# Performance work log

Hardware: AMD Instinct MI355X
Metric: run time of the kernel (lower is better)

The kernel has to match this reference:

```python
import jax, jax.numpy as jnp
import numpy as np

N = 50000      # nodes
E_RAND = 600000  # random edges per meta-path
M = 3          # meta-paths
D_IN = 128
D_OUT = 128
H_SEM = 128    # SemanticAttention hidden (default 128)
NEG_SLOPE = 0.2  # DGL GATConv leaky_relu default


def setup_inputs() -> dict:
    key = jax.random.key(0)
    ks = jax.random.split(key, 12)
    h = jax.random.normal(ks[0], (N, D_IN), dtype=jnp.float32)
    src = jax.random.randint(ks[1], (M, E_RAND), 0, N, dtype=jnp.int32)
    dst = jax.random.randint(ks[2], (M, E_RAND), 0, N, dtype=jnp.int32)
    # add self-loops (dgl.add_self_loop): guarantees every dst has >=1 edge
    loops = jnp.broadcast_to(jnp.arange(N, dtype=jnp.int32), (M, N))
    edge_src = jnp.concatenate([src, loops], axis=1)
    edge_dst = jnp.concatenate([dst, loops], axis=1)
    W_gat = jax.random.normal(ks[3], (M, D_IN, D_OUT), dtype=jnp.float32) * 0.05
    attn_l = jax.random.normal(ks[4], (M, D_OUT), dtype=jnp.float32) * 0.1
    attn_r = jax.random.normal(ks[5], (M, D_OUT), dtype=jnp.float32) * 0.1
    bias_gat = jax.random.normal(ks[6], (M, D_OUT), dtype=jnp.float32) * 0.02
    Ws1 = jax.random.normal(ks[7], (D_OUT, H_SEM), dtype=jnp.float32) * 0.05
    bs1 = jnp.zeros((H_SEM,), dtype=jnp.float32)
    Ws2 = jax.random.normal(ks[8], (H_SEM,), dtype=jnp.float32) * 0.05
    return {"h": h, "edge_src": edge_src, "edge_dst": edge_dst,
            "W_gat": W_gat, "attn_l": attn_l, "attn_r": attn_r,
            "bias_gat": bias_gat, "Ws1": Ws1, "bs1": bs1, "Ws2": Ws2}


def _gat_meta_path(feat_m, el_m, er_m, src, dst):
    # feat_m: [N, D]; el/er: [N]; src/dst: [E]
    e = jax.nn.leaky_relu(el_m[src] + er_m[dst], NEG_SLOPE)  # [E]
    emax = jax.ops.segment_max(e, dst, num_segments=N)       # [N]
    ex = jnp.exp(e - emax[dst])
    denom = jax.ops.segment_sum(ex, dst, num_segments=N)     # [N]
    a = ex / denom[dst]                                      # edge softmax
    # scatter-aggregate weighted source features -> [N, D]
    return jax.ops.segment_sum(a[:, None] * feat_m[src], dst, num_segments=N)


def reference(h, edge_src, edge_dst, W_gat, attn_l, attn_r, bias_gat, Ws1, bs1, Ws2):
    # per-meta-path GATConv projections
    feat = jnp.einsum('ni,mio->mno', h, W_gat)            # [M, N, D]
    el = jnp.einsum('mno,mo->mn', feat, attn_l)           # [M, N]
    er = jnp.einsum('mno,mo->mn', feat, attn_r)           # [M, N]
    z = jax.vmap(_gat_meta_path)(feat, el, er, edge_src, edge_dst)  # [M, N, D]
    z = jax.nn.elu(z + bias_gat[:, None, :])              # GATConv bias + activation
    z = jnp.transpose(z, (1, 0, 2))                       # [N, M, D]
    # SemanticAttention: Linear -> tanh -> Linear(no bias), mean over nodes, softmax over meta-paths
    w = jnp.einsum('nmh,h->nm', jnp.tanh(jnp.einsum('nmd,dh->nmh', z, Ws1) + bs1), Ws2)
    beta = jax.nn.softmax(w.mean(0))                      # [M]
    return jnp.einsum('m,nmd->nd', beta, z)               # [N, D]
```

## Files before the change

### kernel.cpp

```cpp
#include <hip/hip_runtime.h>
#include <hip/hip_fp16.h>

#define NV 50000
#define EE 650000
#define MM 3
#define NBUK 49
#define CHSZ 4096
#define NCH 159
#define SEMBLK 586

typedef __attribute__((ext_vector_type(8))) __bf16 bf16x8;
typedef __attribute__((ext_vector_type(8))) _Float16 f16x8;
typedef __attribute__((ext_vector_type(8))) unsigned short u16x8;
typedef __attribute__((ext_vector_type(4))) float f32x4;

__device__ __forceinline__ unsigned short f2bf(float f) {
    unsigned u = __builtin_bit_cast(unsigned, f);
    u += 0x7FFFu + ((u >> 16) & 1u);
    return (unsigned short)(u >> 16);
}
__device__ __forceinline__ float bflo(unsigned v) {
    unsigned x = v << 16; return __builtin_bit_cast(float, x);
}
__device__ __forceinline__ float bfhi(unsigned v) {
    unsigned x = v & 0xFFFF0000u; return __builtin_bit_cast(float, x);
}
__device__ __forceinline__ bf16x8 zero8() {
    u16x8 u = {0,0,0,0,0,0,0,0};
    return __builtin_bit_cast(bf16x8, u);
}
__device__ __forceinline__ f16x8 zero8h() {
    u16x8 u = {0,0,0,0,0,0,0,0};
    return __builtin_bit_cast(f16x8, u);
}
__device__ __forceinline__ unsigned short f2h(float f) {
    return __builtin_bit_cast(unsigned short, __float2half(f));
}
__device__ __forceinline__ float h2f(unsigned short u) {
    return __half2float(__builtin_bit_cast(__half, u));
}

__global__ void prep_wt(const float* __restrict__ Wg, const float* __restrict__ Ws1,
                        unsigned short* __restrict__ WT, unsigned short* __restrict__ WsT) {
    int idx = blockIdx.x * 256 + threadIdx.x;
    if (idx < MM * 16384) {
        int m = idx / 16384, r = idx % 16384;
        int o = r >> 7, d = r & 127;
        WT[idx] = f2bf(Wg[m * 16384 + d * 128 + o]);
    } else {
        int r = idx - MM * 16384;
        int j = r >> 7, d = r & 127;
        WsT[r] = f2h(Ws1[d * 128 + j]);
    }
}

__global__ void prep_h(const float* __restrict__ h, unsigned* __restrict__ hb) {
    int idx = blockIdx.x * 256 + threadIdx.x;
    if (idx < NV * 64) {
        float2 f = *reinterpret_cast<const float2*>(h + (size_t)idx * 2);
        hb[idx] = ((unsigned)f2bf(f.x)) | (((unsigned)f2bf(f.y)) << 16);
    }
}

__global__ __launch_bounds__(256, 2) void gemm_feat(
    const unsigned short* __restrict__ hb, const unsigned short* __restrict__ WT,
    const float* __restrict__ attn_l, const float* __restrict__ attn_r,
    unsigned* __restrict__ featb, float* __restrict__ el, float* __restrict__ er) {
    const int m = blockIdx.y;
    const int tid = threadIdx.x;
    const int wave = tid >> 6, lane = tid & 63;
    const int lo = lane & 15, hi = lane >> 4;
    const int rowbase = blockIdx.x * 256 + wave * 64;
    const unsigned short* WTm = WT + m * 16384;

    f32x4 acc[4][8];
#pragma unroll
    for (int a = 0; a < 4; ++a)
#pragma unroll
        for (int b = 0; b < 8; ++b) acc[a][b] = (f32x4){0.f, 0.f, 0.f, 0.f};

#pragma unroll
    for (int kk = 0; kk < 4; ++kk) {
        bf16x8 bfrag[8];
#pragma unroll
        for (int ct = 0; ct < 8; ++ct)
            bfrag[ct] = *reinterpret_cast<const bf16x8*>(WTm + (ct * 16 + lo) * 128 + kk * 32 + hi * 8);
#pragma unroll
        for (int rt = 0; rt < 4; ++rt) {
            int row = rowbase + rt * 16 + lo;
            bf16x8 af = (row < NV)
                ? *reinterpret_cast<const bf16x8*>(hb + (size_t)row * 128 + kk * 32 + hi * 8)
                : zero8();
#pragma unroll
            for (int ct = 0; ct < 8; ++ct)
                acc[rt][ct] = __builtin_amdgcn_mfma_f32_16x16x32_bf16(af, bfrag[ct], acc[rt][ct], 0, 0, 0);
        }
    }

    float alv[8], arv[8];
#pragma unroll
    for (int ct = 0; ct < 8; ++ct) {
        alv[ct] = attn_l[m * 128 + ct * 16 + lo];
        arv[ct] = attn_r[m * 128 + ct * 16 + lo];
    }

#pragma unroll
    for (int rt = 0; rt < 4; ++rt) {
        float pl[4] = {0.f, 0.f, 0.f, 0.f}, pr[4] = {0.f, 0.f, 0.f, 0.f};
#pragma unroll
        for (int ct = 0; ct < 8; ++ct)
#pragma unroll
            for (int i = 0; i < 4; ++i) {
                pl[i] += acc[rt][ct][i] * alv[ct];
                pr[i] += acc[rt][ct][i] * arv[ct];
            }
#pragma unroll
        for (int s = 1; s < 16; s <<= 1)
#pragma unroll
            for (int i = 0; i < 4; ++i) {
                pl[i] += __shfl_xor(pl[i], s, 64);
                pr[i] += __shfl_xor(pr[i], s, 64);
            }
        int row0 = rowbase + rt * 16 + hi * 4;
        if (lo == 0) {
#pragma unroll
            for (int i = 0; i < 4; ++i)
                if (row0 + i < NV) {
                    el[m * NV + row0 + i] = pl[i];
                    er[m * NV + row0 + i] = pr[i];
                }
        }
#pragma unroll
        for (int ct = 0; ct < 8; ++ct)
#pragma unroll
            for (int i = 0; i < 4; ++i) {
                float v = acc[rt][ct][i];
                float vp = __shfl_xor(v, 1, 64);
                int row = row0 + i;
                if (((lo & 1) == 0) && row < NV) {
                    unsigned pk = ((unsigned)f2bf(v)) | (((unsigned)f2bf(vp)) << 16);
                    featb[(size_t)(m * NV + row) * 64 + ct * 8 + (lo >> 1)] = pk;
                }
            }
    }
}

__global__ __launch_bounds__(256) void hist_k(const int* __restrict__ edst,
                                              int* __restrict__ counts) {
    int m = blockIdx.y, c = blockIdx.x, tid = threadIdx.x;
    __shared__ int hsm[NBUK];
    if (tid < NBUK) hsm[tid] = 0;
    __syncthreads();
    int base = c * CHSZ;
#pragma unroll
    for (int i = 0; i < CHSZ / 256; ++i) {
        int e = base + i * 256 + tid;
        if (e < EE) {
            int d = edst[(size_t)m * EE + e];
            atomicAdd(&hsm[d >> 10], 1);
        }
    }
    __syncthreads();
    if (tid < NBUK) counts[(m * NCH + c) * NBUK + tid] = hsm[tid];
}

__global__ __launch_bounds__(256) void scan_k(const int* __restrict__ counts,
                                              int* __restrict__ chunkpos,
                                              int* __restrict__ bstart) {
    int t = threadIdx.x;
    __shared__ int btot[MM * NBUK];
    if (t < MM * NBUK) {
        int m = t / NBUK, b = t % NBUK;
        int run = 0;
        for (int c = 0; c < NCH; ++c) {
            chunkpos[(m * NCH + c) * NBUK + b] = run;
            run += counts[(m * NCH + c) * NBUK + b];
        }
        btot[t] = run;
    }
    __syncthreads();
    if (t == 0) {
        for (int m = 0; m < MM; ++m) {
            int run = 0;
            for (int b = 0; b < NBUK; ++b) {
                bstart[m * NBUK + b] = run;
                run += btot[m * NBUK + b];
            }
        }
    }
}

__global__ __launch_bounds__(256) void scat1_k(const int* __restrict__ esrc,
                                               const int* __restrict__ edst,
                                               const int* __restrict__ chunkpos,
                                               const int* __restrict__ bstart,
                                               unsigned* __restrict__ staging) {
    int m = blockIdx.y, c = blockIdx.x, tid = threadIdx.x;
    __shared__ int cnt[NBUK];
    __shared__ int sofs[NBUK];
    if (tid < NBUK) {
        cnt[tid] = 0;
        sofs[tid] = bstart[m * NBUK + tid] + chunkpos[(m * NCH + c) * NBUK + tid];
    }
    __syncthreads();
    int base = c * CHSZ;
#pragma unroll
    for (int i = 0; i < CHSZ / 256; ++i) {
        int e = base + i * 256 + tid;
        if (e < EE) {
            int s = esrc[(size_t)m * EE + e];
            int d = edst[(size_t)m * EE + e];
            int b = d >> 10;
            int r = atomicAdd(&cnt[b], 1);
            staging[(size_t)m * EE + sofs[b] + r] =
                ((unsigned)(d & 1023) << 16) | (unsigned)s;
        }
    }
}

__global__ __launch_bounds__(1024) void bsort_k(const unsigned* __restrict__ staging,
                                                const int* __restrict__ bstart,
                                                const float* __restrict__ el,
                                                const float* __restrict__ er,
                                                unsigned* __restrict__ csr,
                                                int* __restrict__ start,
                                                int* __restrict__ deg) {
    int b = blockIdx.x, m = blockIdx.y, t = threadIdx.x;
    __shared__ int hsm[1024];
    __shared__ int sc[1024];
    __shared__ int cur[1024];
    hsm[t] = 0;
    __syncthreads();
    int sbase = bstart[m * NBUK + b];
    int nseg = ((b == NBUK - 1) ? EE : bstart[m * NBUK + b + 1]) - sbase;
    const unsigned* sp = staging + (size_t)m * EE + sbase;
    for (int i = t; i < nseg; i += 1024)
        atomicAdd(&hsm[sp[i] >> 16], 1);
    __syncthreads();
    int v = hsm[t];
    sc[t] = v;
    __syncthreads();
#pragma unroll
    for (int s = 1; s < 1024; s <<= 1) {
        int add = (t >= s) ? sc[t - s] : 0;
        __syncthreads();
        sc[t] += add;
        __syncthreads();
    }
    int excl = sc[t] - v;
    cur[t] = excl;
    int node = (b << 10) + t;
    if (node < NV) {
        deg[m * NV + node] = v;
        start[m * NV + node] = sbase + excl;
    }
    __syncthreads();
    unsigned* cp = csr + (size_t)m * EE + sbase;
    int node0 = b << 10;
    for (int i = t; i < nseg; i += 1024) {
        unsigned rec = sp[i];
        int dloc = rec >> 16;
        int s = rec & 0xFFFF;
        float x = el[m * NV + s] + er[m * NV + node0 + dloc];
        x = x > 0.f ? x : 0.2f * x;
        float ex = __expf(x);
        int slot = atomicAdd(&cur[dloc], 1);
        cp[slot] = ((unsigned)f2h(ex) << 16) | (unsigned)s;
    }
}

__global__ __launch_bounds__(256) void aggregate_k(
    const unsigned* __restrict__ featb, const unsigned* __restrict__ csr,
    const int* __restrict__ start, const int* __restrict__ deg,
    const float* __restrict__ bias, unsigned* __restrict__ zh) {
    int wid = blockIdx.x * 4 + (threadIdx.x >> 6);
    int gw = wid * 2 + ((threadIdx.x >> 5) & 1);
    int sl = threadIdx.x & 31;
    int m = gw / NV;
    int st = start[gw];
    int dg = deg[gw];
    const unsigned* pp = csr + (size_t)m * EE + st;
    const unsigned* fb = featb + (size_t)m * NV * 64 + sl * 2;
    float2 a01 = {0.f, 0.f}, a23 = {0.f, 0.f};
    float den = 0.f;
    int full = dg & ~7;
    int e0 = 0;
    for (; e0 < full; e0 += 8) {
        unsigned p[8];
#pragma unroll
        for (int i = 0; i < 8; ++i) p[i] = pp[e0 + i];
        uint2 v[8];
#pragma unroll
        for (int i = 0; i < 8; ++i)
            v[i] = *reinterpret_cast<const uint2*>(fb + (size_t)(p[i] & 0xFFFF) * 64);
#pragma unroll
        for (int i = 0; i < 8; ++i) {
            float x = h2f((unsigned short)(p[i] >> 16));
            a01.x += x * bflo(v[i].x); a01.y += x * bfhi(v[i].x);
            a23.x += x * bflo(v[i].y); a23.y += x * bfhi(v[i].y);
            den += x;
        }
    }
    if (e0 < dg) {
        int dgm1 = dg - 1;
        unsigned p[8];
#pragma unroll
        for (int i = 0; i < 8; ++i) p[i] = pp[min(e0 + i, dgm1)];
        uint2 v[8];
#pragma unroll
        for (int i = 0; i < 8; ++i)
            v[i] = *reinterpret_cast<const uint2*>(fb + (size_t)(p[i] & 0xFFFF) * 64);
#pragma unroll
        for (int i = 0; i < 8; ++i) {
            float x = (e0 + i < dg) ? h2f((unsigned short)(p[i] >> 16)) : 0.f;
            a01.x += x * bflo(v[i].x); a01.y += x * bfhi(v[i].x);
            a23.x += x * bflo(v[i].y); a23.y += x * bfhi(v[i].y);
            den += x;
        }
    }
    float inv = 1.f / den;
    int d0 = sl * 4;
    const float* bp = bias + m * 128 + d0;
    float z0 = a01.x * inv + bp[0];
    float z1 = a01.y * inv + bp[1];
    float z2 = a23.x * inv + bp[2];
    float z3 = a23.y * inv + bp[3];
    z0 = z0 > 0.f ? z0 : (__expf(z0) - 1.f);
    z1 = z1 > 0.f ? z1 : (__expf(z1) - 1.f);
    z2 = z2 > 0.f ? z2 : (__expf(z2) - 1.f);
    z3 = z3 > 0.f ? z3 : (__expf(z3) - 1.f);
    uint2 o;
    o.x = ((unsigned)f2h(z0)) | (((unsigned)f2h(z1)) << 16);
    o.y = ((unsigned)f2h(z2)) | (((unsigned)f2h(z3)) << 16);
    *reinterpret_cast<uint2*>(zh + (size_t)gw * 64 + sl * 2) = o;
}

__global__ __launch_bounds__(256, 2) void semantic_k(
    const unsigned* __restrict__ zh, const unsigned short* __restrict__ WsT,
    const float* __restrict__ bs1, const float* __restrict__ Ws2,
    float* __restrict__ wpart) {
    const int tid = threadIdx.x;
    const int wave = tid >> 6, lane = tid & 63;
    const int lo = lane & 15, hi = lane >> 4;
    const int rowbase = blockIdx.x * 256 + wave * 64;

    f32x4 acc[4][8];
#pragma unroll
    for (int a = 0; a < 4; ++a)
#pragma unroll
        for (int b = 0; b < 8; ++b) acc[a][b] = (f32x4){0.f, 0.f, 0.f, 0.f};

#pragma unroll
    for (int kk = 0; kk < 4; ++kk) {
        f16x8 bfrag[8];
#pragma unroll
        for (int ct = 0; ct < 8; ++ct)
            bfrag[ct] = *reinterpret_cast<const f16x8*>(WsT + (ct * 16 + lo) * 128 + kk * 32 + hi * 8);
#pragma unroll
        for (int rt = 0; rt < 4; ++rt) {
            int row = rowbase + rt * 16 + lo;
            f16x8 af = (row < MM * NV)
                ? *reinterpret_cast<const f16x8*>(zh + (size_t)row * 64 + kk * 16 + hi * 2)
                : zero8h();
#pragma unroll
            for (int ct = 0; ct < 8; ++ct)
                acc[rt][ct] = __builtin_amdgcn_mfma_f32_16x16x32_f16(af, bfrag[ct], acc[rt][ct], 0, 0, 0);
        }
    }

    float w2v[8], b1v[8];
#pragma unroll
    for (int ct = 0; ct < 8; ++ct) {
        w2v[ct] = Ws2[ct * 16 + lo];
        b1v[ct] = bs1[ct * 16 + lo];
    }

    float t0 = 0.f, t1 = 0.f, t2 = 0.f;
#pragma unroll
    for (int rt = 0; rt < 4; ++rt) {
        int rbase = rowbase + rt * 16;
        if (rbase >= MM * NV) continue;
        int mm = rbase / NV;
        float p = 0.f;
#pragma unroll
        for (int ct = 0; ct < 8; ++ct)
#pragma unroll
            for (int i = 0; i < 4; ++i) {
                float x = acc[rt][ct][i] + b1v[ct];
                x = fminf(fmaxf(x, -15.f), 15.f);
                float t = __expf(2.f * x);
                p += w2v[ct] * ((t - 1.f) / (t + 1.f));
            }
#pragma unroll
        for (int s = 1; s < 64; s <<= 1) p += __shfl_xor(p, s, 64);
        if (mm == 0) t0 += p; else if (mm == 1) t1 += p; else t2 += p;
    }

    __shared__ float smw[4][3];
    if (lane == 0) { smw[wave][0] = t0; smw[wave][1] = t1; smw[wave][2] = t2; }
    __syncthreads();
    if (tid < 3)
        wpart[blockIdx.x * 4 + tid] =
            smw[0][tid] + smw[1][tid] + smw[2][tid] + smw[3][tid];
}

__global__ __launch_bounds__(64) void beta_k(const float* __restrict__ wpart,
                                             float* __restrict__ beta) {
    int lane = threadIdx.x;
    float t0 = 0.f, t1 = 0.f, t2 = 0.f;
    for (int b = lane; b < SEMBLK; b += 64) {
        t0 += wpart[b * 4 + 0];
        t1 += wpart[b * 4 + 1];
        t2 += wpart[b * 4 + 2];
    }
#pragma unroll
    for (int s = 1; s < 64; s <<= 1) {
        t0 += __shfl_xor(t0, s, 64);
        t1 += __shfl_xor(t1, s, 64);
        t2 += __shfl_xor(t2, s, 64);
    }
    if (lane == 0) {
        float w0 = t0 * (1.f / NV), w1 = t1 * (1.f / NV), w2 = t2 * (1.f / NV);
        float mx = fmaxf(w0, fmaxf(w1, w2));
        float e0 = __expf(w0 - mx), e1 = __expf(w1 - mx), e2 = __expf(w2 - mx);
        float inv = 1.f / (e0 + e1 + e2);
        beta[0] = e0 * inv; beta[1] = e1 * inv; beta[2] = e2 * inv;
    }
}

__global__ __launch_bounds__(256) void combine_k(const unsigned* __restrict__ zh,
                                                 const float* __restrict__ beta,
                                                 float* __restrict__ out) {
    int idx = blockIdx.x * 256 + threadIdx.x;
    float b0 = beta[0], b1 = beta[1], b2 = beta[2];
    uint2 u0 = *reinterpret_cast<const uint2*>(zh + (size_t)idx * 2);
    uint2 u1 = *reinterpret_cast<const uint2*>(zh + (size_t)NV * 64 + (size_t)idx * 2);
    uint2 u2 = *reinterpret_cast<const uint2*>(zh + (size_t)2 * NV * 64 + (size_t)idx * 2);
    float2 a0 = __half22float2(__builtin_bit_cast(__half2, u0.x));
    float2 a1 = __half22float2(__builtin_bit_cast(__half2, u0.y));
    float2 c0 = __half22float2(__builtin_bit_cast(__half2, u1.x));
    float2 c1 = __half22float2(__builtin_bit_cast(__half2, u1.y));
    float2 d0 = __half22float2(__builtin_bit_cast(__half2, u2.x));
    float2 d1 = __half22float2(__builtin_bit_cast(__half2, u2.y));
    float4 o;
    o.x = b0 * a0.x + b1 * c0.x + b2 * d0.x;
    o.y = b0 * a0.y + b1 * c0.y + b2 * d0.y;
    o.z = b0 * a1.x + b1 * c1.x + b2 * d1.x;
    o.w = b0 * a1.y + b1 * c1.y + b2 * d1.y;
    *reinterpret_cast<float4*>(out + (size_t)idx * 4) = o;
}

extern "C" void kernel_launch(void* const* d_in, const int* in_sizes, int n_in,
                              void* d_out, int out_size, void* d_ws, size_t ws_size,
                              hipStream_t stream) {
    const float* h      = (const float*)d_in[0];
    const int*   esrc   = (const int*)d_in[1];
    const int*   edst   = (const int*)d_in[2];
    const float* Wg     = (const float*)d_in[3];
    const float* attn_l = (const float*)d_in[4];
    const float* attn_r = (const float*)d_in[5];
    const float* bias   = (const float*)d_in[6];
    const float* Ws1    = (const float*)d_in[7];
    const float* bs1    = (const float*)d_in[8];
    const float* Ws2    = (const float*)d_in[9];
    float* out = (float*)d_out;

    char* w = (char*)d_ws;
    auto alloc = [&](size_t bytes) { char* p = w; w += (bytes + 255) & ~(size_t)255; return p; };
    unsigned short* WT   = (unsigned short*)alloc((size_t)MM * 128 * 128 * 2);
    unsigned short* WsT  = (unsigned short*)alloc((size_t)128 * 128 * 2);
    unsigned* hb    = (unsigned*)alloc((size_t)NV * 64 * 4);
    unsigned* featb = (unsigned*)alloc((size_t)MM * NV * 64 * 4);
    unsigned* zh    = (unsigned*)alloc((size_t)MM * NV * 64 * 4);
    float* el     = (float*)alloc((size_t)MM * NV * 4);
    float* er     = (float*)alloc((size_t)MM * NV * 4);
    int*   deg    = (int*)alloc((size_t)MM * NV * 4);
    int*   startb = (int*)alloc((size_t)MM * NV * 4);
    int*   counts = (int*)alloc((size_t)MM * NCH * NBUK * 4);
    int*   chunkpos = (int*)alloc((size_t)MM * NCH * NBUK * 4);
    int*   bstart = (int*)alloc((size_t)MM * NBUK * 4);
    unsigned* staging = (unsigned*)alloc((size_t)MM * EE * 4);
    unsigned* csr     = (unsigned*)alloc((size_t)MM * EE * 4);
    float* wpart  = (float*)alloc((size_t)SEMBLK * 4 * 4);
    float* beta   = (float*)alloc(256);

    hipLaunchKernelGGL(prep_wt, dim3(256), dim3(256), 0, stream, Wg, Ws1, WT, WsT);
    hipLaunchKernelGGL(prep_h, dim3((NV * 64 + 255) / 256), dim3(256), 0, stream, h, hb);
    hipLaunchKernelGGL(gemm_feat, dim3(196, MM), dim3(256), 0, stream,
                       (const unsigned short*)hb, WT, attn_l, attn_r, featb, el, er);
    hipLaunchKernelGGL(hist_k, dim3(NCH, MM), dim3(256), 0, stream, edst, counts);
    hipLaunchKernelGGL(scan_k, dim3(1), dim3(256), 0, stream, counts, chunkpos, bstart);
    hipLaunchKernelGGL(scat1_k, dim3(NCH, MM), dim3(256), 0, stream,
                       esrc, edst, chunkpos, bstart, staging);
    hipLaunchKernelGGL(bsort_k, dim3(NBUK, MM), dim3(1024), 0, stream,
                       staging, bstart, el, er, csr, startb, deg);
    hipLaunchKernelGGL(aggregate_k, dim3((MM * NV) / 8), dim3(256), 0, stream,
                       featb, csr, startb, deg, bias, zh);
    hipLaunchKernelGGL(semantic_k, dim3(SEMBLK), dim3(256), 0, stream,
                       zh, WsT, bs1, Ws2, wpart);
    hipLaunchKernelGGL(beta_k, dim3(1), dim3(64), 0, stream, wpart, beta);
    hipLaunchKernelGGL(combine_k, dim3(6250), dim3(256), 0, stream, zh, beta, out);
}
```

Before: 233.5 us.

## Pad CSR segments to multiples of 8, use fp16 features, finer buckets, merged prep

Each node's CSR segment is now padded to a multiple of 8 entries, with zero-weight filler records and aligned per-bucket offsets. This lets the aggregation loop use vectorized uint4 index loads and drop its masked tail iteration. Buckets shrink from 1024 to 256 nodes (196 buckets), so bsort runs more, smaller blocks, and the two prep kernels become one launch. Projected features are stored as fp16 instead of bf16 and accumulated with FMAs. The padding costs extra memory and padded gathers (index 0 with weight 0), and fp16 features carry some overflow/precision risk.

```diff
diff --git a/kernel.cpp b/kernel.cpp
--- a/kernel.cpp
+++ b/kernel.cpp
@@ -4,7 +4,9 @@
 #define NV 50000
 #define EE 650000
 #define MM 3
-#define NBUK 49
+#define NBUK 196
+#define PADCAP 2048
+#define CSRSTRIDE (EE + NBUK * PADCAP)
 #define CHSZ 4096
 #define NCH 159
 #define SEMBLK 586
@@ -19,12 +21,6 @@
     u += 0x7FFFu + ((u >> 16) & 1u);
     return (unsigned short)(u >> 16);
 }
-__device__ __forceinline__ float bflo(unsigned v) {
-    unsigned x = v << 16; return __builtin_bit_cast(float, x);
-}
-__device__ __forceinline__ float bfhi(unsigned v) {
-    unsigned x = v & 0xFFFF0000u; return __builtin_bit_cast(float, x);
-}
 __device__ __forceinline__ bf16x8 zero8() {
     u16x8 u = {0,0,0,0,0,0,0,0};
     return __builtin_bit_cast(bf16x8, u);
@@ -40,25 +36,22 @@
     return __half2float(__builtin_bit_cast(__half, u));
 }
 
-__global__ void prep_wt(const float* __restrict__ Wg, const float* __restrict__ Ws1,
-                        unsigned short* __restrict__ WT, unsigned short* __restrict__ WsT) {
-    int idx = blockIdx.x * 256 + threadIdx.x;
-    if (idx < MM * 16384) {
-        int m = idx / 16384, r = idx % 16384;
-        int o = r >> 7, d = r & 127;
-        WT[idx] = f2bf(Wg[m * 16384 + d * 128 + o]);
-    } else {
-        int r = idx - MM * 16384;
-        int j = r >> 7, d = r & 127;
-        WsT[r] = f2h(Ws1[d * 128 + j]);
-    }
-}
-
-__global__ void prep_h(const float* __restrict__ h, unsigned* __restrict__ hb) {
+__global__ void prep_all(const float* __restrict__ h, const float* __restrict__ Wg,
+                         const float* __restrict__ Ws1, unsigned* __restrict__ hb,
+                         unsigned short* __restrict__ WT, unsigned short* __restrict__ WsT) {
     int idx = blockIdx.x * 256 + threadIdx.x;
     if (idx < NV * 64) {
         float2 f = *reinterpret_cast<const float2*>(h + (size_t)idx * 2);
         hb[idx] = ((unsigned)f2bf(f.x)) | (((unsigned)f2bf(f.y)) << 16);
+    } else if (idx < NV * 64 + MM * 16384) {
+        int r0 = idx - NV * 64;
+        int m = r0 / 16384, r = r0 % 16384;
+        int o = r >> 7, d = r & 127;
+        WT[r0] = f2bf(Wg[m * 16384 + d * 128 + o]);
+    } else {
+        int r = idx - NV * 64 - MM * 16384;
+        int j = r >> 7, d = r & 127;
+        WsT[r] = f2h(Ws1[d * 128 + j]);
     }
 }
 
@@ -138,7 +131,7 @@
                 float vp = __shfl_xor(v, 1, 64);
                 int row = row0 + i;
                 if (((lo & 1) == 0) && row < NV) {
-                    unsigned pk = ((unsigned)f2bf(v)) | (((unsigned)f2bf(vp)) << 16);
+                    unsigned pk = ((unsigned)f2h(v)) | (((unsigned)f2h(vp)) << 16);
                     featb[(size_t)(m * NV + row) * 64 + ct * 8 + (lo >> 1)] = pk;
                 }
             }
@@ -157,16 +150,16 @@
         int e = base + i * 256 + tid;
         if (e < EE) {
             int d = edst[(size_t)m * EE + e];
-            atomicAdd(&hsm[d >> 10], 1);
+            atomicAdd(&hsm[d >> 8], 1);
         }
     }
     __syncthreads();
     if (tid < NBUK) counts[(m * NCH + c) * NBUK + tid] = hsm[tid];
 }
 
-__global__ __launch_bounds__(256) void scan_k(const int* __restrict__ counts,
-                                              int* __restrict__ chunkpos,
-                                              int* __restrict__ bstart) {
+__global__ __launch_bounds__(1024) void scan_k(const int* __restrict__ counts,
+                                               int* __restrict__ chunkpos,
+                                               int* __restrict__ bstart) {
     int t = threadIdx.x;
     __shared__ int btot[MM * NBUK];
     if (t < MM * NBUK) {
@@ -210,54 +203,57 @@
         if (e < EE) {
             int s = esrc[(size_t)m * EE + e];
             int d = edst[(size_t)m * EE + e];
-            int b = d >> 10;
+            int b = d >> 8;
             int r = atomicAdd(&cnt[b], 1);
             staging[(size_t)m * EE + sofs[b] + r] =
-                ((unsigned)(d & 1023) << 16) | (unsigned)s;
-        }
-    }
-}
-
-__global__ __launch_bounds__(1024) void bsort_k(const unsigned* __restrict__ staging,
-                                                const int* __restrict__ bstart,
-                                                const float* __restrict__ el,
-                                                const float* __restrict__ er,
-                                                unsigned* __restrict__ csr,
-                                                int* __restrict__ start,
-                                                int* __restrict__ deg) {
+                ((unsigned)(d & 255) << 16) | (unsigned)s;
+        }
+    }
+}
+
+__global__ __launch_bounds__(256) void bsort_k(const unsigned* __restrict__ staging,
+                                               const int* __restrict__ bstart,
+                                               const float* __restrict__ el,
+                                               const float* __restrict__ er,
+                                               unsigned* __restrict__ csr,
+                                               int* __restrict__ start,
+                                               int* __restrict__ deg) {
     int b = blockIdx.x, m = blockIdx.y, t = threadIdx.x;
-    __shared__ int hsm[1024];
-    __shared__ int sc[1024];
-    __shared__ int cur[1024];
+    __shared__ int hsm[256];
+    __shared__ int sc[256];
+    __shared__ int cur[256];
     hsm[t] = 0;
     __syncthreads();
     int sbase = bstart[m * NBUK + b];
     int nseg = ((b == NBUK - 1) ? EE : bstart[m * NBUK + b + 1]) - sbase;
     const unsigned* sp = staging + (size_t)m * EE + sbase;
-    for (int i = t; i < nseg; i += 1024)
+    for (int i = t; i < nseg; i += 256)
         atomicAdd(&hsm[sp[i] >> 16], 1);
     __syncthreads();
     int v = hsm[t];
-    sc[t] = v;
-    __syncthreads();
-#pragma unroll
-    for (int s = 1; s < 1024; s <<= 1) {
+    int pv = (v + 7) & ~7;
+    sc[t] = pv;
+    __syncthreads();
+#pragma unroll
+    for (int s = 1; s < 256; s <<= 1) {
         int add = (t >= s) ? sc[t - s] : 0;
         __syncthreads();
         sc[t] += add;
         __syncthreads();
     }
-    int excl = sc[t] - v;
-    cur[t] = excl;
-    int node = (b << 10) + t;
+    int pexcl = sc[t] - pv;
+    int pb = ((sbase + 7) & ~7) + b * PADCAP;
+    cur[t] = pb + pexcl;
+    int node = (b << 8) + t;
     if (node < NV) {
-        deg[m * NV + node] = v;
-        start[m * NV + node] = sbase + excl;
-    }
-    __syncthreads();
-    unsigned* cp = csr + (size_t)m * EE + sbase;
-    int node0 = b << 10;
-    for (int i = t; i < nseg; i += 1024) {
+        deg[m * NV + node] = pv;
+        start[m * NV + node] = pb + pexcl;
+    }
+    unsigned* cpm = csr + (size_t)m * CSRSTRIDE;
+    for (int k = v; k < pv; ++k) cpm[pb + pexcl + k] = 0;
+    __syncthreads();
+    int node0 = b << 8;
+    for (int i = t; i < nseg; i += 256) {
         unsigned rec = sp[i];
         int dloc = rec >> 16;
         int s = rec & 0xFFFF;
@@ -265,7 +261,7 @@
         x = x > 0.f ? x : 0.2f * x;
         float ex = __expf(x);
         int slot = atomicAdd(&cur[dloc], 1);
-        cp[slot] = ((unsigned)f2h(ex) << 16) | (unsigned)s;
+        cpm[slot] = ((unsigned)f2h(ex) << 16) | (unsigned)s;
     }
 }
 
@@ -279,16 +275,14 @@
     int m = gw / NV;
     int st = start[gw];
     int dg = deg[gw];
-    const unsigned* pp = csr + (size_t)m * EE + st;
+    const unsigned* pp = csr + (size_t)m * CSRSTRIDE + st;
     const unsigned* fb = featb + (size_t)m * NV * 64 + sl * 2;
-    float2 a01 = {0.f, 0.f}, a23 = {0.f, 0.f};
+    float a0 = 0.f, a1 = 0.f, a2 = 0.f, a3 = 0.f;
     float den = 0.f;
-    int full = dg & ~7;
-    int e0 = 0;
-    for (; e0 < full; e0 += 8) {
-        unsigned p[8];
-#pragma unroll
-        for (int i = 0; i < 8; ++i) p[i] = pp[e0 + i];
+    for (int e0 = 0; e0 < dg; e0 += 8) {
+        uint4 r0 = *reinterpret_cast<const uint4*>(pp + e0);
+        uint4 r1 = *reinterpret_cast<const uint4*>(pp + e0 + 4);
+        unsigned p[8] = {r0.x, r0.y, r0.z, r0.w, r1.x, r1.y, r1.z, r1.w};
         uint2 v[8];
 #pragma unroll
         for (int i = 0; i < 8; ++i)
@@ -296,35 +290,22 @@
 #pragma unroll
         for (int i = 0; i < 8; ++i) {
             float x = h2f((unsigned short)(p[i] >> 16));
-            a01.x += x * bflo(v[i].x); a01.y += x * bfhi(v[i].x);
-            a23.x += x * bflo(v[i].y); a23.y += x * bfhi(v[i].y);
-            den += x;
-        }
-    }
-    if (e0 < dg) {
-        int dgm1 = dg - 1;
-        unsigned p[8];
-#pragma unroll
-        for (int i = 0; i < 8; ++i) p[i] = pp[min(e0 + i, dgm1)];
-        uint2 v[8];
-#pragma unroll
-        for (int i = 0; i < 8; ++i)
-            v[i] = *reinterpret_cast<const uint2*>(fb + (size_t)(p[i] & 0xFFFF) * 64);
-#pragma unroll
-        for (int i = 0; i < 8; ++i) {
-            float x = (e0 + i < dg) ? h2f((unsigned short)(p[i] >> 16)) : 0.f;
-            a01.x += x * bflo(v[i].x); a01.y += x * bfhi(v[i].x);
-            a23.x += x * bflo(v[i].y); a23.y += x * bfhi(v[i].y);
+            __half2 h0 = __builtin_bit_cast(__half2, v[i].x);
+            __half2 h1 = __builtin_bit_cast(__half2, v[i].y);
+            a0 = fmaf(x, __low2float(h0),  a0);
+            a1 = fmaf(x, __high2float(h0), a1);
+            a2 = fmaf(x, __low2float(h1),  a2);
+            a3 = fmaf(x, __high2float(h1), a3);
             den += x;
         }
     }
     float inv = 1.f / den;
     int d0 = sl * 4;
     const float* bp = bias + m * 128 + d0;
-    float z0 = a01.x * inv + bp[0];
-    float z1 = a01.y * inv + bp[1];
-    float z2 = a23.x * inv + bp[2];
-    float z3 = a23.y * inv + bp[3];
+    float z0 = a0 * inv + bp[0];
+    float z1 = a1 * inv + bp[1];
+    float z2 = a2 * inv + bp[2];
+    float z3 = a3 * inv + bp[3];
     z0 = z0 > 0.f ? z0 : (__expf(z0) - 1.f);
     z1 = z1 > 0.f ? z1 : (__expf(z1) - 1.f);
     z2 = z2 > 0.f ? z2 : (__expf(z2) - 1.f);
@@ -480,19 +461,19 @@
     int*   chunkpos = (int*)alloc((size_t)MM * NCH * NBUK * 4);
     int*   bstart = (int*)alloc((size_t)MM * NBUK * 4);
     unsigned* staging = (unsigned*)alloc((size_t)MM * EE * 4);
-    unsigned* csr     = (unsigned*)alloc((size_t)MM * EE * 4);
+    unsigned* csr     = (unsigned*)alloc((size_t)MM * CSRSTRIDE * 4);
     float* wpart  = (float*)alloc((size_t)SEMBLK * 4 * 4);
     float* beta   = (float*)alloc(256);
 
-    hipLaunchKernelGGL(prep_wt, dim3(256), dim3(256), 0, stream, Wg, Ws1, WT, WsT);
-    hipLaunchKernelGGL(prep_h, dim3((NV * 64 + 255) / 256), dim3(256), 0, stream, h, hb);
+    hipLaunchKernelGGL(prep_all, dim3((NV * 64 + (MM + 1) * 16384) / 256), dim3(256), 0, stream,
+                       h, Wg, Ws1, hb, WT, WsT);
     hipLaunchKernelGGL(gemm_feat, dim3(196, MM), dim3(256), 0, stream,
                        (const unsigned short*)hb, WT, attn_l, attn_r, featb, el, er);
     hipLaunchKernelGGL(hist_k, dim3(NCH, MM), dim3(256), 0, stream, edst, counts);
-    hipLaunchKernelGGL(scan_k, dim3(1), dim3(256), 0, stream, counts, chunkpos, bstart);
+    hipLaunchKernelGGL(scan_k, dim3(1), dim3(1024), 0, stream, counts, chunkpos, bstart);
     hipLaunchKernelGGL(scat1_k, dim3(NCH, MM), dim3(256), 0, stream,
                        esrc, edst, chunkpos, bstart, staging);
-    hipLaunchKernelGGL(bsort_k, dim3(NBUK, MM), dim3(1024), 0, stream,
+    hipLaunchKernelGGL(bsort_k, dim3(NBUK, MM), dim3(256), 0, stream,
                        staging, bstart, el, er, csr, startb, deg);
     hipLaunchKernelGGL(aggregate_k, dim3((MM * NV) / 8), dim3(256), 0, stream,
                        featb, csr, startb, deg, bias, zh);
```

Measured after the change: 229.8 us. Within noise of the previous version (-1.6%).
